# Performance work log

Measured on AMD Instinct MI355X. Metric: run time of the kernel, lower is better.

## Reference

```python
import jax, jax.numpy as jnp
import numpy as np

# Dimensions (match init_kwargs / input_specs)
B, C, T, S = 256, 1, 48, 64   # batch, channels, seq_len, input grid side
N = 4                          # lstm_num_square
N2 = N * N
E = 64                         # embedding_size
H = 128                        # hidden_size
DV = 3                         # downsample_version (features per cell)


def setup_inputs() -> dict:
    key = jax.random.key(0)
    ks = jax.random.split(key, 8)
    def rn(k, shape, scale=0.05):
        return jax.random.normal(k, shape, dtype=jnp.float32) * scale
    return {
        "x": jax.random.normal(ks[0], (B, C, T, S, S), dtype=jnp.float32),
        # down_linear_embed: (DV -> E)
        "Wd": rn(ks[1], (DV, E)), "bd": jnp.zeros((E,), jnp.float32),
        # social_linear_embed: (N2*H -> E)
        "Ws": rn(ks[2], (N2 * H, E)), "bs": jnp.zeros((E,), jnp.float32),
        # per-cell LSTMCell weights, stacked over the N2 grid cells (PyTorch layout: [4H, in])
        "W_ih": rn(ks[3], (N2, 4 * H, 2 * E)), "b_ih": jnp.zeros((N2, 4 * H), jnp.float32),
        "W_hh": rn(ks[4], (N2, 4 * H, H)), "b_hh": jnp.zeros((N2, 4 * H), jnp.float32),
        # per-cell linear_ho: (H -> H)
        "W_ho": rn(ks[5], (N2, H, H)), "b_ho": jnp.zeros((N2, H), jnp.float32),
        # out_linear: (H -> 1)
        "W_out": rn(ks[6], (H, 1)), "b_out": jnp.zeros((1,), jnp.float32),
    }


def _downsample(x):
    """DownSampleForLSTM (version 3): channel 0 only; pool the SxS grid into an
    NxN grid of cells, emitting (mean, max, min) per cell -> (T, B, N, N, 3)."""
    blk = S // N
    x0 = x[:, 0]  # (B, T, S, S)
    xb = x0.reshape(B, T, N, blk, N, blk).transpose(0, 1, 2, 4, 3, 5)
    xb = xb.reshape(B, T, N, N, blk * blk)
    feats = jnp.stack([xb.mean(-1), xb.max(-1), xb.min(-1)], axis=-1)  # (B,T,N,N,3)
    return jnp.transpose(feats, (1, 0, 2, 3, 4))  # (T,B,N,N,3)


def reference(x, Wd, bd, Ws, bs, W_ih, b_ih, W_hh, b_hh, W_ho, b_ho, W_out, b_out):
    # Embed downsampled features (dropout is identity in eval mode)
    emb = jax.nn.relu(_downsample(x) @ Wd + bd)         # (T,B,N,N,E)
    emb = emb.reshape(T, B, N2, E)                      # (T,B,N2,E)

    h0 = jnp.zeros((B, N2, H), x.dtype)
    c0 = jnp.zeros((B, N2, H), x.dtype)

    def step(carry, frame):
        h, c = carry  # each (B, N2, H)
        social = jax.nn.relu(h.reshape(B, N2 * H) @ Ws + bs)            # (B,E)
        xt = jnp.concatenate(
            [frame, jnp.broadcast_to(social[:, None, :], (B, N2, E))], axis=-1)  # (B,N2,2E)
        # all N2 LSTMCells at once; g indexes the 4H gate dim
        gates = (jnp.einsum('bne,nge->bng', xt, W_ih)
                 + jnp.einsum('bnh,ngh->bng', h, W_hh)
                 + b_ih + b_hh)                                          # (B,N2,4H)
        i, f, g, o = jnp.split(gates, 4, axis=-1)                        # PyTorch gate order
        c_new = jax.nn.sigmoid(f) * c + jax.nn.sigmoid(i) * jnp.tanh(g)
        h_new = jax.nn.sigmoid(o) * jnp.tanh(c_new)
        out_t = jax.nn.sigmoid(jnp.einsum('bnh,nho->bno', h_new, W_ho) + b_ho)  # (B,N2,H)
        return (h_new, c_new), out_t

    _, outs = jax.lax.scan(step, (h0, c0), emb)   # (T,B,N2,H)
    y = (outs @ W_out + b_out)[..., 0]            # (T,B,N2)
    return y.reshape(T, B, N, N)
```

## Files before the change

kernel.cpp:

```cpp
#include <hip/hip_runtime.h>
#include <hip/hip_cooperative_groups.h>
#include <cmath>

namespace cg = cooperative_groups;


typedef __attribute__((ext_vector_type(8))) short bf16x8;
typedef __attribute__((ext_vector_type(4))) float f32x4;

__device__ __forceinline__ float fexp2(float x){ return __builtin_amdgcn_exp2f(x); }
__device__ __forceinline__ float frcp(float x){ return __builtin_amdgcn_rcpf(x); }
__device__ __forceinline__ float sigf(float x){ return frcp(1.0f + fexp2(-1.44269504f*x)); }
__device__ __forceinline__ float tanh_f(float x){ return 1.0f - 2.0f*frcp(1.0f + fexp2(2.88539008f*x)); }
__device__ __forceinline__ unsigned short f2bf(float f){
  unsigned u = __builtin_bit_cast(unsigned, f);
  return (unsigned short)((u + 0x7FFFu + ((u>>16)&1u)) >> 16);
}
__device__ __forceinline__ int ax(int b, int kb){ return (b<<9) + (kb ^ ((b&7)<<4)); }
__device__ __forceinline__ int axe(int b, int kb){ return (b<<7) + (kb ^ ((b&7)<<4)); }

#define OFF_WOF 0
#define OFF_WSF 32768
#define OFF_XB  49152
#define OFF_EMB 57344
#define OFF_RED 61440
#define SMEM_BYTES 69888

__global__ __launch_bounds__(512, 2) void k_fused(
    const float* __restrict__ x, const float* __restrict__ Wd, const float* __restrict__ bd,
    const float* __restrict__ Ws, const float* __restrict__ bs,
    const float* __restrict__ W_ih, const float* __restrict__ b_ih,
    const float* __restrict__ W_hh, const float* __restrict__ b_hh,
    const float* __restrict__ W_ho, const float* __restrict__ b_ho,
    const float* __restrict__ W_out, const float* __restrict__ b_out,
    float* __restrict__ y,
    unsigned short* __restrict__ emb2b, float* __restrict__ psoc, int* __restrict__ flagv)
{
  extern __shared__ unsigned char smem[];
  unsigned char* sWoF  = smem + OFF_WOF;
  unsigned char* sWsF  = smem + OFF_WSF;
  unsigned char* sXb   = smem + OFF_XB;
  unsigned char* sEmbD = smem + OFF_EMB;
  float* red           = (float*)(smem + OFF_RED);

  const int bid = blockIdx.x, tid = threadIdx.x;
  const int lane = tid & 63, w = tid >> 6;
  cg::grid_group grid = cg::this_grid();

  const int n  = ((bid & 7) << 1) | ((bid >> 3) & 1);
  const int bt = bid >> 4, b0c = bt*16;

  for (int j = tid; j < 192; j += 512)
    __hip_atomic_store(&flagv[(((j>>2)*16 + bt)*64 + n*4 + (j&3))*4], 0,
                       __ATOMIC_RELAXED, __HIP_MEMORY_SCOPE_AGENT);

  {
    const float wd0 = Wd[lane], wd1 = Wd[64+lane], wd2 = Wd[128+lane], bde = bd[lane];
    float* scr = red + w*64;
    for (int it = 0; it < 6; ++it) {
      const int t = w + it*8;
      const float* xp = x + ((size_t)bid*48 + t)*4096;
      #pragma unroll
      for (int ci = 0; ci < 4; ++ci) {
        const float* rp = xp + (16*ci + (lane>>4))*64 + (lane&15)*4;
        float4 a0 = *(const float4*)(rp);
        float4 a1 = *(const float4*)(rp + 256);
        float4 a2 = *(const float4*)(rp + 512);
        float4 a3 = *(const float4*)(rp + 768);
        float sm = a0.x+a0.y+a0.z+a0.w + a1.x+a1.y+a1.z+a1.w
                 + a2.x+a2.y+a2.z+a2.w + a3.x+a3.y+a3.z+a3.w;
        float mx = fmaxf(fmaxf(fmaxf(fmaxf(a0.x,a0.y),fmaxf(a0.z,a0.w)),
                               fmaxf(fmaxf(a1.x,a1.y),fmaxf(a1.z,a1.w))),
                         fmaxf(fmaxf(fmaxf(a2.x,a2.y),fmaxf(a2.z,a2.w)),
                               fmaxf(fmaxf(a3.x,a3.y),fmaxf(a3.z,a3.w))));
        float mn = fminf(fminf(fminf(fminf(a0.x,a0.y),fminf(a0.z,a0.w)),
                               fminf(fminf(a1.x,a1.y),fminf(a1.z,a1.w))),
                         fminf(fminf(fminf(a2.x,a2.y),fminf(a2.z,a2.w)),
                               fminf(fminf(a3.x,a3.y),fminf(a3.z,a3.w))));
        #pragma unroll
        for (int m = 0; m < 4; ++m) {
          const int msk = (m<2) ? (1<<m) : (1<<(m+2));
          sm += __shfl_xor(sm, msk);
          mx = fmaxf(mx, __shfl_xor(mx, msk));
          mn = fminf(mn, __shfl_xor(mn, msk));
        }
        if (lane < 16 && (lane & 3) == 0) {
          int cj = lane >> 2;
          scr[(ci*4+cj)*3+0] = sm * (1.0f/256.0f);
          scr[(ci*4+cj)*3+1] = mx;
          scr[(ci*4+cj)*3+2] = mn;
        }
      }
      #pragma unroll
      for (int cell = 0; cell < 16; ++cell) {
        float vv = scr[cell*3]*wd0 + scr[cell*3+1]*wd1 + scr[cell*3+2]*wd2 + bde;
        emb2b[(((size_t)t*16 + cell)*256 + bid)*64 + lane] = f2bf(fmaxf(vv, 0.f));
      }
    }
  }

  __syncthreads();
  for (int s = tid; s < 1024; s += 512) {
    int wv = s >> 8, kt = (s >> 6) & 3, ln = s & 63;
    int e = wv*16 + (ln & 15), kb = kt*32 + (ln >> 4)*8;
    const float* src = Ws + (size_t)n*8192 + (size_t)kb*64 + e;
    bf16x8 v;
    #pragma unroll
    for (int j = 0; j < 8; ++j) v[j] = (short)f2bf(src[(size_t)j*64]);
    *(bf16x8*)&sWsF[s*16] = v;
  }
  for (int s = tid; s < 2048; s += 512) {
    int wv = s >> 8, kt = (s >> 6) & 3, ln = s & 63;
    int o = wv*16 + (ln & 15), kb = kt*32 + (ln >> 4)*8;
    const float* src = W_ho + (size_t)n*16384 + (size_t)kb*128 + o;
    bf16x8 v;
    #pragma unroll
    for (int j = 0; j < 8; ++j) v[j] = (short)f2bf(src[(size_t)j*128]);
    *(bf16x8*)&sWoF[s*16] = v;
  }

  const int hcol = w*16 + (lane & 15);
  bf16x8 bw[4][8];
  float bias[4];
  {
    const int krow = (lane >> 4)*8;
    #pragma unroll
    for (int G = 0; G < 4; ++G) {
      const float* srcI = W_ih + ((size_t)n*512 + G*128 + hcol)*128;
      const float* srcH = W_hh + ((size_t)n*512 + G*128 + hcol)*128;
      #pragma unroll
      for (int kt = 0; kt < 8; ++kt) {
        const float* s = (kt < 4) ? (srcI + kt*32 + krow) : (srcH + (kt-4)*32 + krow);
        float4 aa = *(const float4*)s;
        float4 bb = *(const float4*)(s+4);
        bf16x8 v;
        v[0]=(short)f2bf(aa.x); v[1]=(short)f2bf(aa.y); v[2]=(short)f2bf(aa.z); v[3]=(short)f2bf(aa.w);
        v[4]=(short)f2bf(bb.x); v[5]=(short)f2bf(bb.y); v[6]=(short)f2bf(bb.z); v[7]=(short)f2bf(bb.w);
        bw[G][kt] = v;
      }
      int gg = n*512 + G*128 + hcol;
      bias[G] = b_ih[gg] + b_hh[gg];
    }
  }
  { int b = tid >> 5, j = tid & 31;
    *(uint2*)&sXb[ax(b, 256 + j*8)] = make_uint2(0u, 0u); }

  asm volatile("s_waitcnt vmcnt(0)" ::: "memory");
  grid.sync();

  const int ocol = w*16 + (lane & 15);
  const float bho = b_ho[n*128 + ocol], wout = W_out[ocol];
  const float bout = b_out[0];
  const int sb = tid >> 5, sj = tid & 31, se2 = sj*2;
  const float bs0 = bs[se2], bs1 = bs[se2+1];
  float creg[4] = {0.f, 0.f, 0.f, 0.f};
  const int ab = lane & 15, akb = (lane >> 4)*16;

  { unsigned v = *(const unsigned*)&emb2b[(((size_t)0*16 + n)*256 + b0c + sb)*64 + se2];
    *(unsigned*)&sEmbD[axe(sb, sj*4)] = v; }
  __syncthreads();

  for (int t = 0; t < 48; ++t) {
    const unsigned char* sEmb = sEmbD + (t&1)*2048;

    f32x4 acc[4];
    #pragma unroll
    for (int G = 0; G < 4; ++G) { f32x4 c0 = {bias[G], bias[G], bias[G], bias[G]}; acc[G] = c0; }
    #pragma unroll
    for (int kt = 0; kt < 2; ++kt) {
      bf16x8 aF = *(const bf16x8*)&sEmb[axe(ab, kt*64 + akb)];
      #pragma unroll
      for (int G = 0; G < 4; ++G)
        acc[G] = __builtin_amdgcn_mfma_f32_16x16x32_bf16(aF, bw[G][kt], acc[G], 0, 0, 0);
    }
    #pragma unroll
    for (int kt = 4; kt < 8; ++kt) {
      bf16x8 aF = *(const bf16x8*)&sXb[ax(ab, kt*64 + akb)];
      #pragma unroll
      for (int G = 0; G < 4; ++G)
        acc[G] = __builtin_amdgcn_mfma_f32_16x16x32_bf16(aF, bw[G][kt], acc[G], 0, 0, 0);
    }

    if (t > 0 && tid < 64) {
      const int* fp = &flagv[(((t-1)*16 + bt)*64 + tid)*4];
      int f0 = __hip_atomic_load(fp, __ATOMIC_RELAXED, __HIP_MEMORY_SCOPE_AGENT);
      while (!f0) {
        __builtin_amdgcn_s_sleep(1);
        f0 = __hip_atomic_load(fp, __ATOMIC_RELAXED, __HIP_MEMORY_SCOPE_AGENT);
      }
    }
    __syncthreads();

    { float s0 = bs0, s1 = bs1;
      if (t > 0) {
        const unsigned long long* pb = (const unsigned long long*)
          (psoc + (size_t)((t-1)&1)*1048576 + (size_t)(b0c + sb)*64 + se2);
        unsigned long long v[16];
        #pragma unroll
        for (int nn = 0; nn < 16; ++nn)
          v[nn] = __hip_atomic_load(pb + (size_t)nn*8192, __ATOMIC_RELAXED, __HIP_MEMORY_SCOPE_AGENT);
        #pragma unroll
        for (int nn = 0; nn < 16; ++nn) {
          float2 f2 = __builtin_bit_cast(float2, v[nn]);
          s0 += f2.x; s1 += f2.y;
        }
      }
      unsigned pk = (unsigned)f2bf(fmaxf(s0,0.f)) | ((unsigned)f2bf(fmaxf(s1,0.f)) << 16);
      *(unsigned*)&sXb[ax(sb, 128 + sj*4)] = pk; }
    __syncthreads();

    #pragma unroll
    for (int kt = 2; kt < 4; ++kt) {
      bf16x8 aF = *(const bf16x8*)&sXb[ax(ab, kt*64 + akb)];
      #pragma unroll
      for (int G = 0; G < 4; ++G)
        acc[G] = __builtin_amdgcn_mfma_f32_16x16x32_bf16(aF, bw[G][kt], acc[G], 0, 0, 0);
    }

    #pragma unroll
    for (int r = 0; r < 4; ++r) {
      int b = (lane >> 4)*4 + r;
      float cn = sigf(acc[1][r])*creg[r] + sigf(acc[0][r])*tanh_f(acc[2][r]);
      float hn = sigf(acc[3][r])*tanh_f(cn);
      creg[r] = cn;
      *(unsigned short*)&sXb[ax(b, 256 + hcol*2)] = f2bf(hn);
    }
    __syncthreads();

    f32x4 ph = {bho, bho, bho, bho};
    f32x4 ps = {0.f, 0.f, 0.f, 0.f};
    #pragma unroll
    for (int kt = 0; kt < 4; ++kt) {
      bf16x8 aH = *(const bf16x8*)&sXb[ax(ab, 256 + kt*64 + akb)];
      bf16x8 bo = *(const bf16x8*)&sWoF[((w*4 + kt)*64 + lane)*16];
      ph = __builtin_amdgcn_mfma_f32_16x16x32_bf16(aH, bo, ph, 0, 0, 0);
      if (w < 4) {
        bf16x8 bs_ = *(const bf16x8*)&sWsF[((w*4 + kt)*64 + lane)*16];
        ps = __builtin_amdgcn_mfma_f32_16x16x32_bf16(aH, bs_, ps, 0, 0, 0);
      }
    }
    if (w < 4 && t < 47) {
      float* pw = psoc + (size_t)(t&1)*1048576 + (size_t)n*16384;
      const int ecol = w*16 + (lane & 15);
      #pragma unroll
      for (int r = 0; r < 4; ++r) {
        int b = b0c + (lane >> 4)*4 + r;
        __hip_atomic_store(&pw[(size_t)b*64 + ecol], ps[r], __ATOMIC_RELAXED, __HIP_MEMORY_SCOPE_AGENT);
      }
      asm volatile("s_waitcnt vmcnt(0)" ::: "memory");
      if (lane == 0)
        __hip_atomic_store(&flagv[((t*16 + bt)*64 + n*4 + w)*4], 1,
                           __ATOMIC_RELAXED, __HIP_MEMORY_SCOPE_AGENT);
    }

    if (t < 47) {
      unsigned v = *(const unsigned*)&emb2b[(((size_t)(t+1)*16 + n)*256 + b0c + sb)*64 + se2];
      *(unsigned*)&sEmbD[((t+1)&1)*2048 + axe(sb, sj*4)] = v;
    }

    #pragma unroll
    for (int r = 0; r < 4; ++r) {
      int b = (lane >> 4)*4 + r;
      red[b*132 + ocol] = wout * sigf(ph[r]);
    }
    __syncthreads();
    if (tid < 256) {
      int bb = tid >> 4, l = tid & 15;
      float sm = 0.f;
      #pragma unroll
      for (int kk = 0; kk < 8; ++kk) sm += red[bb*132 + l + 16*kk];
      #pragma unroll
      for (int m = 8; m >= 1; m >>= 1) sm += __shfl_xor(sm, m, 16);
      if (l == 0) y[((size_t)t*256 + b0c + bb)*16 + n] = sm + bout;
    }
  }
}

extern "C" void kernel_launch(void* const* d_in, const int* in_sizes, int n_in,
                              void* d_out, int out_size, void* d_ws, size_t ws_size,
                              hipStream_t stream){
  const float* x    = (const float*)d_in[0];
  const float* Wd   = (const float*)d_in[1];
  const float* bd   = (const float*)d_in[2];
  const float* Ws   = (const float*)d_in[3];
  const float* bs   = (const float*)d_in[4];
  const float* W_ih = (const float*)d_in[5];
  const float* b_ih = (const float*)d_in[6];
  const float* W_hh = (const float*)d_in[7];
  const float* b_hh = (const float*)d_in[8];
  const float* W_ho = (const float*)d_in[9];
  const float* b_ho = (const float*)d_in[10];
  const float* W_out= (const float*)d_in[11];
  const float* b_out= (const float*)d_in[12];
  float* y = (float*)d_out;

  char* ws = (char*)d_ws;
  unsigned short* emb2b = (unsigned short*)ws;
  float* psoc  = (float*)(ws + 25165824);
  int*   flagv = (int*)(ws + 25165824 + 8388608);

  hipFuncSetAttribute((const void*)k_fused, hipFuncAttributeMaxDynamicSharedMemorySize, SMEM_BYTES);

  void* args[] = { (void*)&x, (void*)&Wd, (void*)&bd, (void*)&Ws, (void*)&bs,
                   (void*)&W_ih, (void*)&b_ih, (void*)&W_hh, (void*)&b_hh,
                   (void*)&W_ho, (void*)&b_ho, (void*)&W_out, (void*)&b_out,
                   (void*)&y, (void*)&emb2b, (void*)&psoc, (void*)&flagv };
  hipLaunchCooperativeKernel((const void*)k_fused, dim3(256), dim3(512), args, SMEM_BYTES, stream);
}
```

Before: 323.3 us.

## Overlap downsample embedding of future frames with the recurrent time loop

```diff
diff --git a/kernel.cpp b/kernel.cpp
--- a/kernel.cpp
+++ b/kernel.cpp
@@ -19,12 +19,13 @@
 __device__ __forceinline__ int ax(int b, int kb){ return (b<<9) + (kb ^ ((b&7)<<4)); }
 __device__ __forceinline__ int axe(int b, int kb){ return (b<<7) + (kb ^ ((b&7)<<4)); }
 
-#define OFF_WOF 0
-#define OFF_WSF 32768
-#define OFF_XB  49152
-#define OFF_EMB 57344
-#define OFF_RED 61440
-#define SMEM_BYTES 69888
+#define OFF_WOF  0
+#define OFF_WSF  32768
+#define OFF_XB   49152
+#define OFF_EMB  57344
+#define OFF_RED  61440
+#define OFF_ESCR 69888
+#define SMEM_BYTES 72192
 
 __global__ __launch_bounds__(512, 2) void k_fused(
     const float* __restrict__ x, const float* __restrict__ Wd, const float* __restrict__ bd,
@@ -50,56 +51,49 @@
   const int n  = ((bid & 7) << 1) | ((bid >> 3) & 1);
   const int bt = bid >> 4, b0c = bt*16;
 
-  for (int j = tid; j < 192; j += 512)
-    __hip_atomic_store(&flagv[(((j>>2)*16 + bt)*64 + n*4 + (j&3))*4], 0,
+  for (int j = tid; j < 384; j += 512)
+    __hip_atomic_store(&flagv[(((j>>3)*16 + bt)*128 + n*8 + (j&7))*4], 0,
                        __ATOMIC_RELAXED, __HIP_MEMORY_SCOPE_AGENT);
 
+  const float wd0 = Wd[lane], wd1 = Wd[64+lane], wd2 = Wd[128+lane], bde = bd[lane];
+
   {
-    const float wd0 = Wd[lane], wd1 = Wd[64+lane], wd2 = Wd[128+lane], bde = bd[lane];
+    const int t2 = w >> 2, cw = w & 3;
+    const float* rp = x + ((size_t)bid*48 + t2)*4096 + (16*cw + (lane>>4))*64 + (lane&15)*4;
+    float4 a0 = *(const float4*)(rp);
+    float4 a1 = *(const float4*)(rp + 256);
+    float4 a2 = *(const float4*)(rp + 512);
+    float4 a3 = *(const float4*)(rp + 768);
+    float sm = a0.x+a0.y+a0.z+a0.w + a1.x+a1.y+a1.z+a1.w
+             + a2.x+a2.y+a2.z+a2.w + a3.x+a3.y+a3.z+a3.w;
+    float mx = fmaxf(fmaxf(fmaxf(fmaxf(a0.x,a0.y),fmaxf(a0.z,a0.w)),
+                           fmaxf(fmaxf(a1.x,a1.y),fmaxf(a1.z,a1.w))),
+                     fmaxf(fmaxf(fmaxf(a2.x,a2.y),fmaxf(a2.z,a2.w)),
+                           fmaxf(fmaxf(a3.x,a3.y),fmaxf(a3.z,a3.w))));
+    float mn = fminf(fminf(fminf(fminf(a0.x,a0.y),fminf(a0.z,a0.w)),
+                           fminf(fminf(a1.x,a1.y),fminf(a1.z,a1.w))),
+                     fminf(fminf(fminf(a2.x,a2.y),fminf(a2.z,a2.w)),
+                           fminf(fminf(a3.x,a3.y),fminf(a3.z,a3.w))));
+    #pragma unroll
+    for (int m = 0; m < 4; ++m) {
+      const int msk = (m<2) ? (1<<m) : (1<<(m+2));
+      sm += __shfl_xor(sm, msk);
+      mx = fmaxf(mx, __shfl_xor(mx, msk));
+      mn = fminf(mn, __shfl_xor(mn, msk));
+    }
     float* scr = red + w*64;
-    for (int it = 0; it < 6; ++it) {
-      const int t = w + it*8;
-      const float* xp = x + ((size_t)bid*48 + t)*4096;
-      #pragma unroll
-      for (int ci = 0; ci < 4; ++ci) {
-        const float* rp = xp + (16*ci + (lane>>4))*64 + (lane&15)*4;
-        float4 a0 = *(const float4*)(rp);
-        float4 a1 = *(const float4*)(rp + 256);
-        float4 a2 = *(const float4*)(rp + 512);
-        float4 a3 = *(const float4*)(rp + 768);
-        float sm = a0.x+a0.y+a0.z+a0.w + a1.x+a1.y+a1.z+a1.w
-                 + a2.x+a2.y+a2.z+a2.w + a3.x+a3.y+a3.z+a3.w;
-        float mx = fmaxf(fmaxf(fmaxf(fmaxf(a0.x,a0.y),fmaxf(a0.z,a0.w)),
-                               fmaxf(fmaxf(a1.x,a1.y),fmaxf(a1.z,a1.w))),
-                         fmaxf(fmaxf(fmaxf(a2.x,a2.y),fmaxf(a2.z,a2.w)),
-                               fmaxf(fmaxf(a3.x,a3.y),fmaxf(a3.z,a3.w))));
-        float mn = fminf(fminf(fminf(fminf(a0.x,a0.y),fminf(a0.z,a0.w)),
-                               fminf(fminf(a1.x,a1.y),fminf(a1.z,a1.w))),
-                         fminf(fminf(fminf(a2.x,a2.y),fminf(a2.z,a2.w)),
-                               fminf(fminf(a3.x,a3.y),fminf(a3.z,a3.w))));
-        #pragma unroll
-        for (int m = 0; m < 4; ++m) {
-          const int msk = (m<2) ? (1<<m) : (1<<(m+2));
-          sm += __shfl_xor(sm, msk);
-          mx = fmaxf(mx, __shfl_xor(mx, msk));
-          mn = fminf(mn, __shfl_xor(mn, msk));
-        }
-        if (lane < 16 && (lane & 3) == 0) {
-          int cj = lane >> 2;
-          scr[(ci*4+cj)*3+0] = sm * (1.0f/256.0f);
-          scr[(ci*4+cj)*3+1] = mx;
-          scr[(ci*4+cj)*3+2] = mn;
-        }
-      }
-      #pragma unroll
-      for (int cell = 0; cell < 16; ++cell) {
-        float vv = scr[cell*3]*wd0 + scr[cell*3+1]*wd1 + scr[cell*3+2]*wd2 + bde;
-        emb2b[(((size_t)t*16 + cell)*256 + bid)*64 + lane] = f2bf(fmaxf(vv, 0.f));
-      }
-    }
-  }
-
+    if (lane < 16 && (lane & 3) == 0) {
+      int cj = lane >> 2;
+      scr[cj*3+0] = sm * (1.0f/256.0f); scr[cj*3+1] = mx; scr[cj*3+2] = mn;
+    }
+    #pragma unroll
+    for (int cj = 0; cj < 4; ++cj) {
+      float vv = scr[cj*3]*wd0 + scr[cj*3+1]*wd1 + scr[cj*3+2]*wd2 + bde;
+      emb2b[(((size_t)t2*16 + 4*cw+cj)*256 + bid)*64 + lane] = f2bf(fmaxf(vv, 0.f));
+    }
+  }
   __syncthreads();
+
   for (int s = tid; s < 1024; s += 512) {
     int wv = s >> 8, kt = (s >> 6) & 3, ln = s & 63;
     int e = wv*16 + (ln & 15), kb = kt*32 + (ln >> 4)*8;
@@ -155,6 +149,7 @@
   const float bs0 = bs[se2], bs1 = bs[se2+1];
   float creg[4] = {0.f, 0.f, 0.f, 0.f};
   const int ab = lane & 15, akb = (lane >> 4)*16;
+  unsigned long long* emb64 = (unsigned long long*)emb2b;
 
   { unsigned v = *(const unsigned*)&emb2b[(((size_t)0*16 + n)*256 + b0c + sb)*64 + se2];
     *(unsigned*)&sEmbD[axe(sb, sj*4)] = v; }
@@ -163,6 +158,16 @@
   for (int t = 0; t < 48; ++t) {
     const unsigned char* sEmb = sEmbD + (t&1)*2048;
 
+    float4 xa0, xa1, xa2, xa3;
+    const bool doEmb = (w >= 4) && (t < 46);
+    if (doEmb) {
+      const float* rp = x + ((size_t)bid*48 + (t+2))*4096 + (16*(w-4) + (lane>>4))*64 + (lane&15)*4;
+      xa0 = *(const float4*)(rp);
+      xa1 = *(const float4*)(rp + 256);
+      xa2 = *(const float4*)(rp + 512);
+      xa3 = *(const float4*)(rp + 768);
+    }
+
     f32x4 acc[4];
     #pragma unroll
     for (int G = 0; G < 4; ++G) { f32x4 c0 = {bias[G], bias[G], bias[G], bias[G]}; acc[G] = c0; }
@@ -181,8 +186,8 @@
         acc[G] = __builtin_amdgcn_mfma_f32_16x16x32_bf16(aF, bw[G][kt], acc[G], 0, 0, 0);
     }
 
-    if (t > 0 && tid < 64) {
-      const int* fp = &flagv[(((t-1)*16 + bt)*64 + tid)*4];
+    if (t > 0 && tid < 128) {
+      const int* fp = &flagv[(((t-1)*16 + bt)*128 + tid)*4];
       int f0 = __hip_atomic_load(fp, __ATOMIC_RELAXED, __HIP_MEMORY_SCOPE_AGENT);
       while (!f0) {
         __builtin_amdgcn_s_sleep(1);
@@ -227,29 +232,78 @@
     }
     __syncthreads();
 
+    bf16x8 aH[4];
+    #pragma unroll
+    for (int kt = 0; kt < 4; ++kt)
+      aH[kt] = *(const bf16x8*)&sXb[ax(ab, 256 + kt*64 + akb)];
+
+    if (w < 4) {
+      f32x4 ps = {0.f, 0.f, 0.f, 0.f};
+      #pragma unroll
+      for (int kt = 0; kt < 4; ++kt) {
+        bf16x8 bs_ = *(const bf16x8*)&sWsF[((w*4 + kt)*64 + lane)*16];
+        ps = __builtin_amdgcn_mfma_f32_16x16x32_bf16(aH[kt], bs_, ps, 0, 0, 0);
+      }
+      if (t < 47) {
+        float* pw = psoc + (size_t)(t&1)*1048576 + (size_t)n*16384;
+        const int ecol = w*16 + (lane & 15);
+        #pragma unroll
+        for (int r = 0; r < 4; ++r) {
+          int b = b0c + (lane >> 4)*4 + r;
+          __hip_atomic_store(&pw[(size_t)b*64 + ecol], ps[r], __ATOMIC_RELAXED, __HIP_MEMORY_SCOPE_AGENT);
+        }
+      }
+    } else if (doEmb) {
+      float sm = xa0.x+xa0.y+xa0.z+xa0.w + xa1.x+xa1.y+xa1.z+xa1.w
+               + xa2.x+xa2.y+xa2.z+xa2.w + xa3.x+xa3.y+xa3.z+xa3.w;
+      float mx = fmaxf(fmaxf(fmaxf(fmaxf(xa0.x,xa0.y),fmaxf(xa0.z,xa0.w)),
+                             fmaxf(fmaxf(xa1.x,xa1.y),fmaxf(xa1.z,xa1.w))),
+                       fmaxf(fmaxf(fmaxf(xa2.x,xa2.y),fmaxf(xa2.z,xa2.w)),
+                             fmaxf(fmaxf(xa3.x,xa3.y),fmaxf(xa3.z,xa3.w))));
+      float mn = fminf(fminf(fminf(fminf(xa0.x,xa0.y),fminf(xa0.z,xa0.w)),
+                             fminf(fminf(xa1.x,xa1.y),fminf(xa1.z,xa1.w))),
+                       fminf(fminf(fminf(xa2.x,xa2.y),fminf(xa2.z,xa2.w)),
+                             fminf(fminf(xa3.x,xa3.y),fminf(xa3.z,xa3.w))));
+      #pragma unroll
+      for (int m = 0; m < 4; ++m) {
+        const int msk = (m<2) ? (1<<m) : (1<<(m+2));
+        sm += __shfl_xor(sm, msk);
+        mx = fmaxf(mx, __shfl_xor(mx, msk));
+        mn = fminf(mn, __shfl_xor(mn, msk));
+      }
+      float* scrS = (float*)(smem + OFF_ESCR + (size_t)(w-4)*576);
+      unsigned short* scrP = (unsigned short*)(smem + OFF_ESCR + (size_t)(w-4)*576 + 64);
+      if (lane < 16 && (lane & 3) == 0) {
+        int cj = lane >> 2;
+        scrS[cj*3+0] = sm * (1.0f/256.0f); scrS[cj*3+1] = mx; scrS[cj*3+2] = mn;
+      }
+      #pragma unroll
+      for (int cj = 0; cj < 4; ++cj) {
+        float vv = scrS[cj*3]*wd0 + scrS[cj*3+1]*wd1 + scrS[cj*3+2]*wd2 + bde;
+        scrP[cj*64 + lane] = f2bf(fmaxf(vv, 0.f));
+      }
+      unsigned long long u = *(const unsigned long long*)&scrP[lane*4];
+      const int cell = 4*(w-4) + (lane >> 4);
+      const size_t dst = (((size_t)(t+2)*16 + cell)*256 + bid)*16 + (lane & 15);
+      __hip_atomic_store(&emb64[dst], u, __ATOMIC_RELAXED, __HIP_MEMORY_SCOPE_AGENT);
+    }
+
     f32x4 ph = {bho, bho, bho, bho};
-    f32x4 ps = {0.f, 0.f, 0.f, 0.f};
     #pragma unroll
     for (int kt = 0; kt < 4; ++kt) {
-      bf16x8 aH = *(const bf16x8*)&sXb[ax(ab, 256 + kt*64 + akb)];
       bf16x8 bo = *(const bf16x8*)&sWoF[((w*4 + kt)*64 + lane)*16];
-      ph = __builtin_amdgcn_mfma_f32_16x16x32_bf16(aH, bo, ph, 0, 0, 0);
-      if (w < 4) {
-        bf16x8 bs_ = *(const bf16x8*)&sWsF[((w*4 + kt)*64 + lane)*16];
-        ps = __builtin_amdgcn_mfma_f32_16x16x32_bf16(aH, bs_, ps, 0, 0, 0);
-      }
-    }
-    if (w < 4 && t < 47) {
-      float* pw = psoc + (size_t)(t&1)*1048576 + (size_t)n*16384;
-      const int ecol = w*16 + (lane & 15);
-      #pragma unroll
-      for (int r = 0; r < 4; ++r) {
-        int b = b0c + (lane >> 4)*4 + r;
-        __hip_atomic_store(&pw[(size_t)b*64 + ecol], ps[r], __ATOMIC_RELAXED, __HIP_MEMORY_SCOPE_AGENT);
-      }
+      ph = __builtin_amdgcn_mfma_f32_16x16x32_bf16(aH[kt], bo, ph, 0, 0, 0);
+    }
+    #pragma unroll
+    for (int r = 0; r < 4; ++r) {
+      int b = (lane >> 4)*4 + r;
+      red[b*132 + ocol] = wout * sigf(ph[r]);
+    }
+
+    if (t < 47) {
       asm volatile("s_waitcnt vmcnt(0)" ::: "memory");
       if (lane == 0)
-        __hip_atomic_store(&flagv[((t*16 + bt)*64 + n*4 + w)*4], 1,
+        __hip_atomic_store(&flagv[((t*16 + bt)*128 + n*8 + w)*4], 1,
                            __ATOMIC_RELAXED, __HIP_MEMORY_SCOPE_AGENT);
     }
 
@@ -258,20 +312,15 @@
       *(unsigned*)&sEmbD[((t+1)&1)*2048 + axe(sb, sj*4)] = v;
     }
 
-    #pragma unroll
-    for (int r = 0; r < 4; ++r) {
-      int b = (lane >> 4)*4 + r;
-      red[b*132 + ocol] = wout * sigf(ph[r]);
-    }
     __syncthreads();
     if (tid < 256) {
       int bb = tid >> 4, l = tid & 15;
-      float sm = 0.f;
-      #pragma unroll
-      for (int kk = 0; kk < 8; ++kk) sm += red[bb*132 + l + 16*kk];
-      #pragma unroll
-      for (int m = 8; m >= 1; m >>= 1) sm += __shfl_xor(sm, m, 16);
-      if (l == 0) y[((size_t)t*256 + b0c + bb)*16 + n] = sm + bout;
+      float sm2 = 0.f;
+      #pragma unroll
+      for (int kk = 0; kk < 8; ++kk) sm2 += red[bb*132 + l + 16*kk];
+      #pragma unroll
+      for (int m = 8; m >= 1; m >>= 1) sm2 += __shfl_xor(sm2, m, 16);
+      if (l == 0) y[((size_t)t*256 + b0c + bb)*16 + n] = sm2 + bout;
     }
   }
 }
```

New measurement: 427.2 us. +32.1%, slower.

## Reorder recurrent step to publish social partials early and defer output reduction

Applied to the files above, without the earlier changes.

```diff
diff --git a/kernel.cpp b/kernel.cpp
--- a/kernel.cpp
+++ b/kernel.cpp
@@ -60,13 +60,18 @@
     for (int it = 0; it < 6; ++it) {
       const int t = w + it*8;
       const float* xp = x + ((size_t)bid*48 + t)*4096;
+      float4 xv[4][4];
       #pragma unroll
       for (int ci = 0; ci < 4; ++ci) {
         const float* rp = xp + (16*ci + (lane>>4))*64 + (lane&15)*4;
-        float4 a0 = *(const float4*)(rp);
-        float4 a1 = *(const float4*)(rp + 256);
-        float4 a2 = *(const float4*)(rp + 512);
-        float4 a3 = *(const float4*)(rp + 768);
+        xv[ci][0] = *(const float4*)(rp);
+        xv[ci][1] = *(const float4*)(rp + 256);
+        xv[ci][2] = *(const float4*)(rp + 512);
+        xv[ci][3] = *(const float4*)(rp + 768);
+      }
+      #pragma unroll
+      for (int ci = 0; ci < 4; ++ci) {
+        float4 a0 = xv[ci][0], a1 = xv[ci][1], a2 = xv[ci][2], a3 = xv[ci][3];
         float sm = a0.x+a0.y+a0.z+a0.w + a1.x+a1.y+a1.z+a1.w
                  + a2.x+a2.y+a2.z+a2.w + a3.x+a3.y+a3.z+a3.w;
         float mx = fmaxf(fmaxf(fmaxf(fmaxf(a0.x,a0.y),fmaxf(a0.z,a0.w)),
@@ -163,6 +168,11 @@
   for (int t = 0; t < 48; ++t) {
     const unsigned char* sEmb = sEmbD + (t&1)*2048;
 
+    if (t < 47) {
+      unsigned v = *(const unsigned*)&emb2b[(((size_t)(t+1)*16 + n)*256 + b0c + sb)*64 + se2];
+      *(unsigned*)&sEmbD[((t+1)&1)*2048 + axe(sb, sj*4)] = v;
+    }
+
     f32x4 acc[4];
     #pragma unroll
     for (int G = 0; G < 4; ++G) { f32x4 c0 = {bias[G], bias[G], bias[G], bias[G]}; acc[G] = c0; }
@@ -192,13 +202,24 @@
     __syncthreads();
 
     { float s0 = bs0, s1 = bs1;
+      unsigned long long v[16];
       if (t > 0) {
         const unsigned long long* pb = (const unsigned long long*)
           (psoc + (size_t)((t-1)&1)*1048576 + (size_t)(b0c + sb)*64 + se2);
-        unsigned long long v[16];
         #pragma unroll
         for (int nn = 0; nn < 16; ++nn)
           v[nn] = __hip_atomic_load(pb + (size_t)nn*8192, __ATOMIC_RELAXED, __HIP_MEMORY_SCOPE_AGENT);
+      }
+      if (t > 0 && tid < 256) {
+        int bb = tid >> 4, l = tid & 15;
+        float sm2 = 0.f;
+        #pragma unroll
+        for (int kk = 0; kk < 8; ++kk) sm2 += red[bb*132 + l + 16*kk];
+        #pragma unroll
+        for (int m = 8; m >= 1; m >>= 1) sm2 += __shfl_xor(sm2, m, 16);
+        if (l == 0) y[((size_t)(t-1)*256 + b0c + bb)*16 + n] = sm2 + bout;
+      }
+      if (t > 0) {
         #pragma unroll
         for (int nn = 0; nn < 16; ++nn) {
           float2 f2 = __builtin_bit_cast(float2, v[nn]);
@@ -227,52 +248,55 @@
     }
     __syncthreads();
 
+    bf16x8 aH[4];
+    #pragma unroll
+    for (int kt = 0; kt < 4; ++kt)
+      aH[kt] = *(const bf16x8*)&sXb[ax(ab, 256 + kt*64 + akb)];
+
+    if (w < 4) {
+      f32x4 ps = {0.f, 0.f, 0.f, 0.f};
+      #pragma unroll
+      for (int kt = 0; kt < 4; ++kt) {
+        bf16x8 bs_ = *(const bf16x8*)&sWsF[((w*4 + kt)*64 + lane)*16];
+        ps = __builtin_amdgcn_mfma_f32_16x16x32_bf16(aH[kt], bs_, ps, 0, 0, 0);
+      }
+      if (t < 47) {
+        float* pw = psoc + (size_t)(t&1)*1048576 + (size_t)n*16384;
+        const int ecol = w*16 + (lane & 15);
+        #pragma unroll
+        for (int r = 0; r < 4; ++r) {
+          int b = b0c + (lane >> 4)*4 + r;
+          __hip_atomic_store(&pw[(size_t)b*64 + ecol], ps[r], __ATOMIC_RELAXED, __HIP_MEMORY_SCOPE_AGENT);
+        }
+        asm volatile("s_waitcnt vmcnt(0)" ::: "memory");
+        if (lane == 0)
+          __hip_atomic_store(&flagv[((t*16 + bt)*64 + n*4 + w)*4], 1,
+                             __ATOMIC_RELAXED, __HIP_MEMORY_SCOPE_AGENT);
+      }
+    }
+
     f32x4 ph = {bho, bho, bho, bho};
-    f32x4 ps = {0.f, 0.f, 0.f, 0.f};
     #pragma unroll
     for (int kt = 0; kt < 4; ++kt) {
-      bf16x8 aH = *(const bf16x8*)&sXb[ax(ab, 256 + kt*64 + akb)];
       bf16x8 bo = *(const bf16x8*)&sWoF[((w*4 + kt)*64 + lane)*16];
-      ph = __builtin_amdgcn_mfma_f32_16x16x32_bf16(aH, bo, ph, 0, 0, 0);
-      if (w < 4) {
-        bf16x8 bs_ = *(const bf16x8*)&sWsF[((w*4 + kt)*64 + lane)*16];
-        ps = __builtin_amdgcn_mfma_f32_16x16x32_bf16(aH, bs_, ps, 0, 0, 0);
-      }
-    }
-    if (w < 4 && t < 47) {
-      float* pw = psoc + (size_t)(t&1)*1048576 + (size_t)n*16384;
-      const int ecol = w*16 + (lane & 15);
-      #pragma unroll
-      for (int r = 0; r < 4; ++r) {
-        int b = b0c + (lane >> 4)*4 + r;
-        __hip_atomic_store(&pw[(size_t)b*64 + ecol], ps[r], __ATOMIC_RELAXED, __HIP_MEMORY_SCOPE_AGENT);
-      }
-      asm volatile("s_waitcnt vmcnt(0)" ::: "memory");
-      if (lane == 0)
-        __hip_atomic_store(&flagv[((t*16 + bt)*64 + n*4 + w)*4], 1,
-                           __ATOMIC_RELAXED, __HIP_MEMORY_SCOPE_AGENT);
-    }
-
-    if (t < 47) {
-      unsigned v = *(const unsigned*)&emb2b[(((size_t)(t+1)*16 + n)*256 + b0c + sb)*64 + se2];
-      *(unsigned*)&sEmbD[((t+1)&1)*2048 + axe(sb, sj*4)] = v;
-    }
-
+      ph = __builtin_amdgcn_mfma_f32_16x16x32_bf16(aH[kt], bo, ph, 0, 0, 0);
+    }
     #pragma unroll
     for (int r = 0; r < 4; ++r) {
       int b = (lane >> 4)*4 + r;
       red[b*132 + ocol] = wout * sigf(ph[r]);
     }
-    __syncthreads();
-    if (tid < 256) {
-      int bb = tid >> 4, l = tid & 15;
-      float sm = 0.f;
-      #pragma unroll
-      for (int kk = 0; kk < 8; ++kk) sm += red[bb*132 + l + 16*kk];
-      #pragma unroll
-      for (int m = 8; m >= 1; m >>= 1) sm += __shfl_xor(sm, m, 16);
-      if (l == 0) y[((size_t)t*256 + b0c + bb)*16 + n] = sm + bout;
-    }
+  }
+
+  __syncthreads();
+  if (tid < 256) {
+    int bb = tid >> 4, l = tid & 15;
+    float sm2 = 0.f;
+    #pragma unroll
+    for (int kk = 0; kk < 8; ++kk) sm2 += red[bb*132 + l + 16*kk];
+    #pragma unroll
+    for (int m = 8; m >= 1; m >>= 1) sm2 += __shfl_xor(sm2, m, 16);
+    if (l == 0) y[((size_t)47*256 + b0c + bb)*16 + n] = sm2 + bout;
   }
 }
 
```

After: 314.4 us. -2.7%, faster.
